# Performance work log

Hardware: AMD Instinct MI355X
Metric: run time of the kernel (lower is better)

The kernel has to match this reference:

```python
import jax, jax.numpy as jnp
import numpy as np

N = 16384      # number of points
DIM = 128      # feature dim
POS_DIM = 3
K = 16         # neighbors (init kwarg k)
SCALE = np.float32(np.sqrt(DIM))


def setup_inputs() -> dict:
    key = jax.random.key(0)
    ks = jax.random.split(key, 16)
    g = lambda i, shape: (jax.random.normal(ks[i], shape, dtype=jnp.float32) * 0.05)
    return {
        "x": jax.random.normal(ks[0], (N, DIM), dtype=jnp.float32),
        "pos": jax.random.uniform(ks[1], (N, POS_DIM), dtype=jnp.float32),
        # weights stored as (in, out); torch Linear applies x @ W.T + b
        "Wq": g(2, (DIM, DIM)),
        "Wk": g(3, (DIM, DIM)),
        "Wv": g(4, (DIM, DIM)),
        "mid_w1": g(5, (DIM, DIM)), "mid_b1": g(6, (DIM,)),
        "mid_w2": g(7, (DIM, DIM)), "mid_b2": g(8, (DIM,)),
        "pe_w1": g(9, (POS_DIM, DIM)), "pe_b1": g(10, (DIM,)),
        "pe_w2": g(11, (DIM, DIM)), "pe_b2": g(12, (DIM,)),
        "fin_w": g(13, (DIM, DIM)), "fin_b": g(14, (DIM,)),
    }


def _knn_indices(pos):
    # squared pairwise distances [N, N]; top-K smallest -> neighbor indices [N, K]
    sq = jnp.sum(pos * pos, axis=-1)
    d2 = sq[:, None] + sq[None, :] - 2.0 * (pos @ pos.T)
    _, ind = jax.lax.top_k(-d2, K)
    return ind


def reference(x, pos, Wq, Wk, Wv, mid_w1, mid_b1, mid_w2, mid_b2,
              pe_w1, pe_b1, pe_w2, pe_b2, fin_w, fin_b):
    ind = _knn_indices(pos)                    # [N, K] int32 (constant wrt grads)
    x_k = x[ind]                               # [N, K, D]
    pos_k = pos[ind]                           # [N, K, 3]
    rel = pos[:, None, :] - pos_k              # [N, K, 3]
    pe = jax.nn.relu(rel @ pe_w1 + pe_b1) @ pe_w2 + pe_b2    # [N, K, D]
    q = x @ Wq                                 # [N, D]
    h = q[:, None, :] - (x_k @ Wk) + pe        # [N, K, D]
    y = jax.nn.relu(h @ mid_w1 + mid_b1) @ mid_w2 + mid_b2   # [N, K, D]
    y = jax.nn.softmax(y / SCALE, axis=-2)     # softmax over neighbors K
    z = x_k @ Wv + pe                          # [N, K, D]
    agg = jnp.sum(y * z, axis=-2)              # [N, D]
    return agg @ fin_w + fin_b + x
```

## Files before the change

kernel.cpp:

```cpp
#include <hip/hip_runtime.h>
#include <hip/hip_bf16.h>

#define N_PTS 16384
#define DIMF  128
#define KNB   16
#define GRES  8
#define NCELL (GRES*GRES*GRES)

typedef __attribute__((ext_vector_type(8))) short bf16x8;
typedef __attribute__((ext_vector_type(4))) short bf16x4;
typedef __attribute__((ext_vector_type(4))) float f32x4;
typedef __attribute__((ext_vector_type(4))) unsigned int u32x4;
typedef __attribute__((ext_vector_type(2))) unsigned int u32x2;

__device__ __forceinline__ unsigned short f2b(float f){
  unsigned int u = __float_as_uint(f);
  u = u + 0x7fffu + ((u >> 16) & 1u);
  return (unsigned short)(u >> 16);
}
__device__ __forceinline__ unsigned cvtpk(float lo, float hi){
  unsigned r;
  asm("v_cvt_pk_bf16_f32 %0, %1, %2" : "=v"(r) : "v"(lo), "v"(hi));
  return r;
}
__device__ __forceinline__ float b2f(unsigned short u){
  return __uint_as_float(((unsigned)u) << 16);
}
__device__ __forceinline__ float b2fs(short s){
  return __uint_as_float(((unsigned)(unsigned short)s) << 16);
}
__device__ __forceinline__ float unsort_f(unsigned s){
  unsigned u = (s & 0x80000000u) ? (s ^ 0x80000000u) : ~s;
  return __uint_as_float(u);
}

__global__ __launch_bounds__(256) void count_kernel(const float* __restrict__ pos, int* __restrict__ cnt){
  int i = blockIdx.x*256 + threadIdx.x;
  float px = pos[i*3+0], py = pos[i*3+1], pz = pos[i*3+2];
  int cx = min(GRES-1, max(0,(int)(px*(float)GRES)));
  int cy = min(GRES-1, max(0,(int)(py*(float)GRES)));
  int cz = min(GRES-1, max(0,(int)(pz*(float)GRES)));
  atomicAdd(&cnt[(cz*GRES+cy)*GRES+cx], 1);
}

__global__ __launch_bounds__(256) void scan_kernel(const int* __restrict__ cnt, int* __restrict__ starts, int* __restrict__ fillp){
  __shared__ int wsum[4];
  int t = threadIdx.x;
  int lane = t & 63, w = t >> 6;
  int a = cnt[2*t], b = cnt[2*t+1];
  int s = a + b;
  int p = s;
  #pragma unroll
  for (int off = 1; off < 64; off <<= 1){
    int v = __shfl_up(p, off, 64);
    if (lane >= off) p += v;
  }
  if (lane == 63) wsum[w] = p;
  __syncthreads();
  int base = 0;
  for (int i = 0; i < w; ++i) base += wsum[i];
  int excl = base + p - s;
  starts[2*t]   = excl;     fillp[2*t]   = excl;
  starts[2*t+1] = excl + a; fillp[2*t+1] = excl + a;
}

__global__ __launch_bounds__(256) void scatter_pack(const float* __restrict__ pos, int* __restrict__ fillp,
                                                    float4* __restrict__ pos4, int* __restrict__ pidx,
                                                    int* __restrict__ inv,
                                                    const float* __restrict__ w0, const float* __restrict__ w1,
                                                    const float* __restrict__ w2, const float* __restrict__ w3,
                                                    const float* __restrict__ w4, const float* __restrict__ w5,
                                                    const float* __restrict__ w6,
                                                    short* __restrict__ dst){
  if (blockIdx.x < 64){
    int i = blockIdx.x*256 + threadIdx.x;
    float px = pos[i*3+0], py = pos[i*3+1], pz = pos[i*3+2];
    int cx = min(GRES-1, max(0,(int)(px*(float)GRES)));
    int cy = min(GRES-1, max(0,(int)(py*(float)GRES)));
    int cz = min(GRES-1, max(0,(int)(pz*(float)GRES)));
    int c = (cz*GRES+cy)*GRES+cx;
    float sq = __fadd_rn(__fadd_rn(__fmul_rn(px,px), __fmul_rn(py,py)), __fmul_rn(pz,pz));
    int s = atomicAdd(&fillp[c], 1);
    pos4[s] = make_float4(px, py, pz, sq);
    pidx[s] = i;
    inv[i] = s;
  } else {
    int pb = blockIdx.x - 64;
    int slot = pb >> 6;
    const float* src = (slot==0)?w0:(slot==1)?w1:(slot==2)?w2:(slot==3)?w3:(slot==4)?w4:(slot==5)?w5:w6;
    int f = (pb & 63)*256 + threadIdx.x;
    int j  = f & 7;
    int ln = (f >> 3) & 63;
    int ks = (f >> 9) & 3;
    int nt = f >> 11;
    int k = ks*32 + ((ln >> 4) << 3) + j;
    int n = nt*16 + (ln & 15);
    dst[slot*16384 + f] = (short)f2b(src[k*DIMF + n]);
  }
}

__global__ __launch_bounds__(256) void knn_query64(const float4* __restrict__ pos4, const int* __restrict__ pidx,
                                                   const int* __restrict__ starts, const int* __restrict__ cnt,
                                                   const int* __restrict__ inv,
                                                   int* __restrict__ ind_slot){
  __shared__ unsigned long long cand[4][64];
  int lane = threadIdx.x & 63;
  int wv   = threadIdx.x >> 6;
  int t = blockIdx.x*4 + wv;
  float4 qp = pos4[t];
  float qx = qp.x, qy = qp.y, qz = qp.z, qsq = qp.w;
  int cx = min(GRES-1, max(0,(int)(qx*(float)GRES)));
  int cy = min(GRES-1, max(0,(int)(qy*(float)GRES)));
  int cz = min(GRES-1, max(0,(int)(qz*(float)GRES)));
  int zlo = max(0,cz-1), zhi = min(GRES-1,cz+1);
  int ylo = max(0,cy-1), yhi = min(GRES-1,cy+1);
  int xlo = max(0,cx-1), xhi = min(GRES-1,cx+1);
  const double h = 0.125;
  double dqx=(double)qx, dqy=(double)qy, dqz=(double)qz;

  int nb = 0;
  if (lane < 27){
    int dz = lane/9 - 1, dy = (lane/3)%3 - 1, dx = lane%3 - 1;
    int zz = cz+dz, yy = cy+dy, xx = cx+dx;
    if (zz>=zlo && zz<=zhi && yy>=ylo && yy<=yhi && xx>=xlo && xx<=xhi)
      nb = cnt[(zz*GRES+yy)*GRES+xx];
  }
  #pragma unroll
  for (int o=1;o<64;o<<=1) nb += __shfl_xor(nb, o, 64);
  float V = (float)((zhi-zlo+1)*(yhi-ylo+1)*(xhi-xlo+1)) * 0.001953125f;
  float r3 = 3.8197186f * V / (float)nb;
  float tau2 = 2.0f * __powf(r3, 0.66666667f);

  int nfound = 0;
  bool okscan = false;
  for (int it = 0; it < 8; ++it){
    nfound = 0;
    for (int zz=zlo; zz<=zhi; ++zz)
    for (int yy=ylo; yy<=yhi; ++yy)
    for (int xx=xlo; xx<=xhi; ++xx){
      double mdx = fmax(0.0, fmax((double)xx*h - dqx, dqx - (double)(xx+1)*h));
      double mdy = fmax(0.0, fmax((double)yy*h - dqy, dqy - (double)(yy+1)*h));
      double mdz = fmax(0.0, fmax((double)zz*h - dqz, dqz - (double)(zz+1)*h));
      double md2 = mdx*mdx + mdy*mdy + mdz*mdz;
      if (md2 > (double)tau2 + 1.0e-5) continue;
      int c = (zz*GRES+yy)*GRES+xx;
      int s0 = starts[c], n = cnt[c];
      for (int b = 0; b < n; b += 64){
        int o = b + lane;
        bool valid = o < n;
        float d = 3.0e38f; int idx = 0;
        if (valid){
          float4 pc = pos4[s0+o];
          idx = pidx[s0+o];
          float dot = __fmaf_rn(qz, pc.z, __fmaf_rn(qy, pc.y, __fmul_rn(qx, pc.x)));
          d   = __fsub_rn(__fadd_rn(qsq, pc.w), __fmul_rn(2.0f, dot));
        }
        bool admit = valid && (d < tau2);
        unsigned long long mask = __ballot(admit);
        if (admit){
          int pos = nfound + (int)__popcll(mask & ((1ull<<lane)-1ull));
          if (pos < 64){
            unsigned su = __float_as_uint(d);
            su ^= (unsigned)((int)su >> 31) | 0x80000000u;
            cand[wv][pos] = ((unsigned long long)su << 32) | (unsigned)idx;
          }
        }
        nfound += (int)__popcll(mask);
      }
    }
    if (nfound > 64){ tau2 *= 0.7f; continue; }
    if (nfound < 16){ tau2 *= 2.0f; continue; }
    okscan = true; break;
  }

  bool needfb = !okscan;
  if (okscan){
    asm volatile("s_waitcnt lgkmcnt(0)" ::: "memory");
    __builtin_amdgcn_sched_barrier(0);
    unsigned long long key = (lane < nfound) ? cand[wv][lane] : ~0ull;

    #pragma unroll
    for (int k = 2; k <= 64; k <<= 1){
      #pragma unroll
      for (int j = k>>1; j >= 1; j >>= 1){
        unsigned long long other = __shfl_xor(key, j, 64);
        bool takeSmall = (((lane & k) == 0) != ((lane & j) != 0));
        bool less = other < key;
        key = (takeSmall == less) ? other : key;
      }
    }
    if (lane < 16) ind_slot[t*KNB + lane] = inv[(int)(unsigned)(key & 0xffffffffu)];

    unsigned long long k15 = __shfl(key, 15, 64);
    float b16 = unsort_f((unsigned)(k15 >> 32));
    double mg = 1.0e300;
    if (cx-1 > 0)      mg = fmin(mg, dqx - (double)(cx-1)*h);
    if (cx+1 < GRES-1) mg = fmin(mg, (double)(cx+2)*h - dqx);
    if (cy-1 > 0)      mg = fmin(mg, dqy - (double)(cy-1)*h);
    if (cy+1 < GRES-1) mg = fmin(mg, (double)(cy+2)*h - dqy);
    if (cz-1 > 0)      mg = fmin(mg, dqz - (double)(cz-1)*h);
    if (cz+1 < GRES-1) mg = fmin(mg, (double)(cz+2)*h - dqz);
    needfb = !(mg*mg > (double)b16 + 1.0e-5);
  }

  if (needfb){
    float bd[KNB]; int bi[KNB];
    #pragma unroll
    for (int k=0;k<KNB;++k){ bd[k] = 3.0e38f; bi[k] = 0x7fffffff; }
    for (int r = 0; r < GRES; ++r){
      int zl = max(0, cz-r), zh = min(GRES-1, cz+r);
      int yl = max(0, cy-r), yh = min(GRES-1, cy+r);
      int xl = max(0, cx-r), xh = min(GRES-1, cx+r);
      for (int zz = zl; zz <= zh; ++zz)
      for (int yy = yl; yy <= yh; ++yy)
      for (int xx = xl; xx <= xh; ++xx){
        int ring = max(abs(zz-cz), max(abs(yy-cy), abs(xx-cx)));
        if (ring != r) continue;
        int c = (zz*GRES+yy)*GRES+xx;
        int s0 = starts[c], e = s0 + cnt[c];
        for (int s = s0; s < e; ++s){
          float4 pc = pos4[s];
          int idx = pidx[s];
          float dot = __fmaf_rn(qz, pc.z, __fmaf_rn(qy, pc.y, __fmul_rn(qx, pc.x)));
          float d   = __fsub_rn(__fadd_rn(qsq, pc.w), __fmul_rn(2.0f, dot));
          bool adm = (d < bd[KNB-1]) || (d == bd[KNB-1] && idx < bi[KNB-1]);
          if (adm){
            #pragma unroll
            for (int p = KNB-1; p >= 1; --p){
              float pd = bd[p-1]; int pi = bi[p-1];
              bool sh  = (pd > d) || (pd == d && pi > idx);
              bool ins = (!sh) && ((bd[p] > d) || (bd[p] == d && bi[p] > idx));
              bd[p] = sh ? pd : (ins ? d   : bd[p]);
              bi[p] = sh ? pi : (ins ? idx : bi[p]);
            }
            bool s0b = (bd[0] > d) || (bd[0] == d && bi[0] > idx);
            if (s0b){ bd[0] = d; bi[0] = idx; }
          }
        }
      }
      if (bd[KNB-1] < 3.0e37f){
        double mg = 1.0e300;
        if (cx - r > 0)      mg = fmin(mg, dqx - (double)(cx-r)*h);
        if (cx + r < GRES-1) mg = fmin(mg, (double)(cx+r+1)*h - dqx);
        if (cy - r > 0)      mg = fmin(mg, dqy - (double)(cy-r)*h);
        if (cy + r < GRES-1) mg = fmin(mg, (double)(cy+r+1)*h - dqy);
        if (cz - r > 0)      mg = fmin(mg, dqz - (double)(cz-r)*h);
        if (cz + r < GRES-1) mg = fmin(mg, (double)(cz+r+1)*h - dqz);
        if (mg*mg > (double)bd[KNB-1] + 1.0e-5) break;
      }
    }
    if (lane < 16) ind_slot[t*KNB + lane] = inv[bi[lane]];
  }
}

__global__ __launch_bounds__(256) void proj_kernel(const float* __restrict__ x, const int* __restrict__ pidx,
                                                   const short* __restrict__ pw,
                                                   unsigned short* __restrict__ q, unsigned short* __restrict__ xk,
                                                   unsigned short* __restrict__ xv){
  __shared__ __align__(16) char Abuf[8192];
  int tid = threadIdx.x, lane = tid & 63, wv = tid >> 6;
  int r0 = blockIdx.x * 32;
  {
    int row = tid >> 3, seg = tid & 7;
    int orig = pidx[r0 + row];
    const float4* xr = (const float4*)(x + (size_t)orig*DIMF + seg*16);
    float4 a = xr[0], b = xr[1], c = xr[2], d = xr[3];
    u32x4 u0, u1;
    u0[0] = cvtpk(a.x, a.y); u0[1] = cvtpk(a.z, a.w);
    u0[2] = cvtpk(b.x, b.y); u0[3] = cvtpk(b.z, b.w);
    u1[0] = cvtpk(c.x, c.y); u1[1] = cvtpk(c.z, c.w);
    u1[2] = cvtpk(d.x, d.y); u1[3] = cvtpk(d.z, d.w);
    *(u32x4*)(&Abuf[row*256 + ((seg*32 +  0) ^ ((row&7)<<4))]) = u0;
    *(u32x4*)(&Abuf[row*256 + ((seg*32 + 16) ^ ((row&7)<<4))]) = u1;
  }
  __syncthreads();
  int mt = wv >> 1;
  int nh = (wv & 1) * 4;
  #pragma unroll 1
  for (int w = 0; w < 3; ++w){
    const bf16x8* bw = (const bf16x8*)(pw + w*16384);
    unsigned short* dst = (w==0) ? q : (w==1) ? xk : xv;
    f32x4 acc[4];
    #pragma unroll
    for (int n=0;n<4;++n) acc[n] = (f32x4){0.f,0.f,0.f,0.f};
    #pragma unroll
    for (int ks=0;ks<4;++ks){
      int ra = mt*16 + (lane&15);
      int cb = ks*64 + ((lane>>4)<<4);
      bf16x8 a0 = *(const bf16x8*)(&Abuf[ra*256 + (cb ^ ((ra&7)<<4))]);
      #pragma unroll
      for (int n=0;n<4;++n){
        bf16x8 b = bw[((nh+n)*4+ks)*64 + lane];
        acc[n] = __builtin_amdgcn_mfma_f32_16x16x32_bf16(a0, b, acc[n], 0, 0, 0);
      }
    }
    #pragma unroll
    for (int n=0;n<4;++n){
      int grow = r0 + mt*16 + ((lane>>4)<<2);
      int col = (nh+n)*16 + (lane&15);
      unsigned pk01 = cvtpk(acc[n][0], acc[n][1]);
      unsigned pk23 = cvtpk(acc[n][2], acc[n][3]);
      dst[(size_t)(grow+0)*DIMF + col] = (unsigned short)pk01;
      dst[(size_t)(grow+1)*DIMF + col] = (unsigned short)(pk01 >> 16);
      dst[(size_t)(grow+2)*DIMF + col] = (unsigned short)pk23;
      dst[(size_t)(grow+3)*DIMF + col] = (unsigned short)(pk23 >> 16);
    }
  }
}

__global__ __launch_bounds__(512, 2) void main_kernel(
    const float* __restrict__ x, const float4* __restrict__ pos4, const int* __restrict__ pidx,
    const float* __restrict__ pe_w1, const float* __restrict__ pe_b1, const float* __restrict__ pe_b2,
    const float* __restrict__ mid_b1, const float* __restrict__ mid_b2, const float* __restrict__ fin_b,
    const unsigned short* __restrict__ qarr, const unsigned short* __restrict__ xkarr,
    const unsigned short* __restrict__ xvarr,
    const int* __restrict__ ind_slot, const short* __restrict__ pw,
    float* __restrict__ out)
{
  __shared__ __align__(16) char peLDS[32768];
  __shared__ __align__(16) char wbuf[32768];
  __shared__ float aggT[DIMF][9];
  __shared__ int indbuf[128];
  __shared__ int origbuf[8];
  int tid = threadIdx.x;
  int lane = tid & 63;
  int wv = tid >> 6;
  int swz = (blockIdx.x & 7) * (N_PTS/8/8) + (blockIdx.x >> 3);
  int t0 = swz * 8;

  int g = lane >> 4, kl = lane & 15;
  int mt = wv;

  #define STAGE_W(slot) { \
    const char* gsrc = (const char*)(pw + (size_t)(slot)*16384) + wv*4096 + lane*16; \
    char* ldst = &wbuf[wv*4096]; \
    __builtin_amdgcn_global_load_lds(gsrc,        ldst,        16, 0, 0); \
    __builtin_amdgcn_global_load_lds(gsrc + 1024, ldst + 1024, 16, 0, 0); \
    __builtin_amdgcn_global_load_lds(gsrc + 2048, ldst + 2048, 16, 0, 0); \
    __builtin_amdgcn_global_load_lds(gsrc + 3072, ldst + 3072, 16, 0, 0); }

  if (tid < 128) indbuf[tid] = ind_slot[swz*128 + tid];
  if (tid < 8) origbuf[tid] = pidx[t0 + tid];
  STAGE_W(3);
  __syncthreads();

  int nb4[4];
  #pragma unroll
  for (int r=0;r<4;++r) nb4[r] = indbuf[mt*16 + g*4 + r];
  int nbr = indbuf[mt*16 + kl];
  unsigned short zraw[8][4];
  #pragma unroll
  for (int nt=0;nt<8;++nt)
    #pragma unroll
    for (int r=0;r<4;++r)
      zraw[nt][r] = xvarr[(size_t)nb4[r]*DIMF + nt*16 + kl];

  bf16x8 tfrag[4];
  {
    float4 pq = pos4[t0+mt];
    float4 pn = pos4[nbr];
    float rx = pq.x-pn.x, ry = pq.y-pn.y, rz = pq.z-pn.z;
    #pragma unroll
    for (int ks=0;ks<4;++ks){
      int c0 = ks*32 + g*8;
      const float4* w0 = (const float4*)(pe_w1 + c0);
      const float4* w1 = (const float4*)(pe_w1 + DIMF + c0);
      const float4* w2 = (const float4*)(pe_w1 + 2*DIMF + c0);
      const float4* bb = (const float4*)(pe_b1 + c0);
      float4 wa0=w0[0], wa1=w0[1], wb0=w1[0], wb1=w1[1], wc0=w2[0], wc1=w2[1], wd0=bb[0], wd1=bb[1];
      float wa[8]={wa0.x,wa0.y,wa0.z,wa0.w,wa1.x,wa1.y,wa1.z,wa1.w};
      float wb[8]={wb0.x,wb0.y,wb0.z,wb0.w,wb1.x,wb1.y,wb1.z,wb1.w};
      float wc[8]={wc0.x,wc0.y,wc0.z,wc0.w,wc1.x,wc1.y,wc1.z,wc1.w};
      float wd[8]={wd0.x,wd0.y,wd0.z,wd0.w,wd1.x,wd1.y,wd1.z,wd1.w};
      float tv[8];
      #pragma unroll
      for (int j=0;j<8;++j)
        tv[j] = fmaxf(fmaf(rx, wa[j], fmaf(ry, wb[j], fmaf(rz, wc[j], wd[j]))), 0.f);
      u32x4 u;
      u[0] = cvtpk(tv[0], tv[1]); u[1] = cvtpk(tv[2], tv[3]);
      u[2] = cvtpk(tv[4], tv[5]); u[3] = cvtpk(tv[6], tv[7]);
      tfrag[ks] = __builtin_bit_cast(bf16x8, u);
    }
  }

  f32x4 acc[8];
  const bf16x8* bw = (const bf16x8*)wbuf;

  {
    #pragma unroll
    for (int nt=0;nt<8;++nt){
      float bv = pe_b2[nt*16 + kl];
      acc[nt] = (f32x4){bv,bv,bv,bv};
    }
    #pragma unroll
    for (int ks=0;ks<4;++ks){
      #pragma unroll
      for (int nt=0;nt<8;++nt){
        bf16x8 b = bw[(nt*4+ks)*64 + lane];
        acc[nt] = __builtin_amdgcn_mfma_f32_16x16x32_bf16(tfrag[ks], b, acc[nt], 0, 0, 0);
      }
    }
  }

  bf16x4 zb[8];
  int r0w = mt*16 + g*4;
  #pragma unroll
  for (int nt=0;nt<8;++nt){
    int col = nt*16 + kl;
    float p0 = acc[nt][0], p1 = acc[nt][1], p2 = acc[nt][2], p3 = acc[nt][3];
    unsigned pk01 = cvtpk(p0, p1), pk23 = cvtpk(p2, p3);
    *(unsigned short*)&peLDS[(r0w+0)*256 + ((col*2) ^ (((r0w+0)&7)<<4))] = (unsigned short)pk01;
    *(unsigned short*)&peLDS[(r0w+1)*256 + ((col*2) ^ (((r0w+1)&7)<<4))] = (unsigned short)(pk01 >> 16);
    *(unsigned short*)&peLDS[(r0w+2)*256 + ((col*2) ^ (((r0w+2)&7)<<4))] = (unsigned short)pk23;
    *(unsigned short*)&peLDS[(r0w+3)*256 + ((col*2) ^ (((r0w+3)&7)<<4))] = (unsigned short)(pk23 >> 16);
    float z0 = b2f(zraw[nt][0]) + p0;
    float z1 = b2f(zraw[nt][1]) + p1;
    float z2 = b2f(zraw[nt][2]) + p2;
    float z3 = b2f(zraw[nt][3]) + p3;
    u32x2 zu; zu[0] = cvtpk(z0, z1); zu[1] = cvtpk(z2, z3);
    zb[nt] = __builtin_bit_cast(bf16x4, zu);
  }

  bf16x8 q8[4], k8[4];
  {
    const unsigned short* qrow = qarr + (size_t)(t0+mt)*DIMF;
    const unsigned short* krow = xkarr + (size_t)nbr*DIMF;
    #pragma unroll
    for (int ks=0;ks<4;++ks){
      int c0 = ks*32 + g*8;
      q8[ks] = *(const bf16x8*)(qrow + c0);
      k8[ks] = *(const bf16x8*)(krow + c0);
    }
  }
  __syncthreads();
  STAGE_W(4);

  bf16x8 hfrag[4];
  {
    int row = mt*16 + kl;
    #pragma unroll
    for (int ks=0;ks<4;++ks){
      int c0 = ks*32 + g*8;
      bf16x8 p8 = *(const bf16x8*)(&peLDS[row*256 + ((c0*2) ^ ((row&7)<<4))]);
      float hf[8];
      #pragma unroll
      for (int j=0;j<8;++j)
        hf[j] = (b2fs(q8[ks][j]) - b2fs(k8[ks][j])) + b2fs(p8[j]);
      u32x4 u;
      u[0] = cvtpk(hf[0], hf[1]); u[1] = cvtpk(hf[2], hf[3]);
      u[2] = cvtpk(hf[4], hf[5]); u[3] = cvtpk(hf[6], hf[7]);
      hfrag[ks] = __builtin_bit_cast(bf16x8, u);
    }
  }
  __syncthreads();

  {
    #pragma unroll
    for (int nt=0;nt<8;++nt){
      float bv = mid_b1[nt*16 + kl];
      acc[nt] = (f32x4){bv,bv,bv,bv};
    }
    #pragma unroll
    for (int ks=0;ks<4;++ks){
      #pragma unroll
      for (int nt=0;nt<8;++nt){
        bf16x8 b = bw[(nt*4+ks)*64 + lane];
        acc[nt] = __builtin_amdgcn_mfma_f32_16x16x32_bf16(hfrag[ks], b, acc[nt], 0, 0, 0);
      }
    }
  }
  __syncthreads();
  STAGE_W(5);
  #pragma unroll
  for (int nt=0;nt<8;++nt){
    int col = nt*16 + kl;
    unsigned pk01 = cvtpk(fmaxf(acc[nt][0],0.f), fmaxf(acc[nt][1],0.f));
    unsigned pk23 = cvtpk(fmaxf(acc[nt][2],0.f), fmaxf(acc[nt][3],0.f));
    *(unsigned short*)&peLDS[(r0w+0)*256 + ((col*2) ^ (((r0w+0)&7)<<4))] = (unsigned short)pk01;
    *(unsigned short*)&peLDS[(r0w+1)*256 + ((col*2) ^ (((r0w+1)&7)<<4))] = (unsigned short)(pk01 >> 16);
    *(unsigned short*)&peLDS[(r0w+2)*256 + ((col*2) ^ (((r0w+2)&7)<<4))] = (unsigned short)pk23;
    *(unsigned short*)&peLDS[(r0w+3)*256 + ((col*2) ^ (((r0w+3)&7)<<4))] = (unsigned short)(pk23 >> 16);
  }
  __syncthreads();

  {
    #pragma unroll
    for (int nt=0;nt<8;++nt){
      float bv = mid_b2[nt*16 + kl];
      acc[nt] = (f32x4){bv,bv,bv,bv};
    }
    #pragma unroll
    for (int ks=0;ks<4;++ks){
      int ra = mt*16 + kl;
      int cb = ks*64 + g*16;
      bf16x8 a0 = *(const bf16x8*)(&peLDS[ra*256 + (cb ^ ((ra&7)<<4))]);
      #pragma unroll
      for (int nt=0;nt<8;++nt){
        bf16x8 b = bw[(nt*4+ks)*64 + lane];
        acc[nt] = __builtin_amdgcn_mfma_f32_16x16x32_bf16(a0, b, acc[nt], 0, 0, 0);
      }
    }
  }
  __syncthreads();
  STAGE_W(6);

  {
    const float invS = 0.08838834764831843f;
    #pragma unroll
    for (int nt=0;nt<8;++nt){
      f32x4 y = acc[nt];
      float mx = fmaxf(fmaxf(y[0],y[1]), fmaxf(y[2],y[3]));
      mx = fmaxf(mx, __shfl_xor(mx, 16, 64));
      mx = fmaxf(mx, __shfl_xor(mx, 32, 64));
      float e0 = __expf((y[0]-mx)*invS);
      float e1 = __expf((y[1]-mx)*invS);
      float e2 = __expf((y[2]-mx)*invS);
      float e3 = __expf((y[3]-mx)*invS);
      float ssum = e0+e1+e2+e3;
      ssum += __shfl_xor(ssum, 16, 64);
      ssum += __shfl_xor(ssum, 32, 64);
      bf16x4 zv = zb[nt];
      float ps = (e0*b2fs(zv[0]) + e1*b2fs(zv[1]) + e2*b2fs(zv[2]) + e3*b2fs(zv[3])) / ssum;
      ps += __shfl_xor(ps, 16, 64);
      ps += __shfl_xor(ps, 32, 64);
      if (lane < 16) aggT[nt*16 + lane][mt] = ps;
    }
  }
  __syncthreads();

  {
    f32x4 facc = (f32x4){0.f,0.f,0.f,0.f};
    #pragma unroll
    for (int ks=0;ks<4;++ks){
      int c0 = ks*32 + g*8;
      float av[8];
      #pragma unroll
      for (int j=0;j<8;++j)
        av[j] = (kl < 8) ? aggT[c0+j][kl] : 0.f;
      u32x4 u;
      u[0] = cvtpk(av[0], av[1]); u[1] = cvtpk(av[2], av[3]);
      u[2] = cvtpk(av[4], av[5]); u[3] = cvtpk(av[6], av[7]);
      bf16x8 a = __builtin_bit_cast(bf16x8, u);
      bf16x8 b = bw[(wv*4+ks)*64 + lane];
      facc = __builtin_amdgcn_mfma_f32_16x16x32_bf16(a, b, facc, 0, 0, 0);
    }
    int col = wv*16 + kl;
    float fb = fin_b[col];
    if (g < 2){
      #pragma unroll
      for (int r=0;r<4;++r){
        int prow = g*4 + r;
        int o = origbuf[prow];
        out[(size_t)o*DIMF + col] = facc[r] + fb + x[(size_t)o*DIMF + col];
      }
    }
  }
  #undef STAGE_W
}

extern "C" void kernel_launch(void* const* d_in, const int* in_sizes, int n_in,
                              void* d_out, int out_size, void* d_ws, size_t ws_size,
                              hipStream_t stream)
{
  (void)in_sizes; (void)n_in; (void)out_size; (void)ws_size;
  const float* x      = (const float*)d_in[0];
  const float* pos    = (const float*)d_in[1];
  const float* Wq     = (const float*)d_in[2];
  const float* Wk     = (const float*)d_in[3];
  const float* Wv     = (const float*)d_in[4];
  const float* mid_w1 = (const float*)d_in[5];
  const float* mid_b1 = (const float*)d_in[6];
  const float* mid_w2 = (const float*)d_in[7];
  const float* mid_b2 = (const float*)d_in[8];
  const float* pe_w1  = (const float*)d_in[9];
  const float* pe_b1  = (const float*)d_in[10];
  const float* pe_w2  = (const float*)d_in[11];
  const float* pe_b2  = (const float*)d_in[12];
  const float* fin_w  = (const float*)d_in[13];
  const float* fin_b  = (const float*)d_in[14];
  float* out = (float*)d_out;
  char* ws = (char*)d_ws;

  int*    cellcnt = (int*)   (ws + 0);
  int*    fillp   = (int*)   (ws + 4096);
  int*    starts  = (int*)   (ws + 8192);
  int*    pidx    = (int*)   (ws + 49152);
  float4* pos4    = (float4*)(ws + 114688);
  int*    ind     = (int*)   (ws + 376832);
  short*  pw      = (short*) (ws + 1425408);
  int*    inv     = (int*)   (ws + 1654784);
  unsigned short* qarr  = (unsigned short*)(ws + 1720320);
  unsigned short* xkarr = (unsigned short*)(ws + 5914624);
  unsigned short* xvarr = (unsigned short*)(ws + 10108928);

  hipMemsetAsync(cellcnt, 0, NCELL*sizeof(int), stream);
  count_kernel  <<<N_PTS/256, 256, 0, stream>>>(pos, cellcnt);
  scan_kernel   <<<1,         256, 0, stream>>>(cellcnt, starts, fillp);
  scatter_pack  <<<64 + 7*64, 256, 0, stream>>>(pos, fillp, pos4, pidx, inv,
                                                Wq, Wk, Wv, pe_w2, mid_w1, mid_w2, fin_w, pw);
  knn_query64   <<<N_PTS/4,   256, 0, stream>>>(pos4, pidx, starts, cellcnt, inv, ind);
  proj_kernel   <<<N_PTS/32,  256, 0, stream>>>(x, pidx, pw, qarr, xkarr, xvarr);
  main_kernel   <<<N_PTS/8,   512, 0, stream>>>(x, pos4, pidx, pe_w1, pe_b1, pe_b2, mid_b1, mid_b2, fin_b,
                                                qarr, xkarr, xvarr, ind, pw, out);
}
```

Before: 157.2 us.

## Fuse grid-based kNN search into main kernel, removing separate kNN launch

The grid-cell kNN query is moved from its own kernel into the start of main_kernel. Each of the 8 waves finds the neighbours for one query point and writes the indices straight into the LDS index buffer, instead of writing them to global memory for a later reload. This removes one kernel launch and the global round trip of the neighbour index array. In exchange, main_kernel takes on the kNN register and control-flow load and 4KB more LDS, which may lower occupancy and lengthen the main kernel's prologue.

```diff
diff --git a/kernel.cpp b/kernel.cpp
--- a/kernel.cpp
+++ b/kernel.cpp
@@ -99,160 +99,6 @@
   }
 }
 
-__global__ __launch_bounds__(256) void knn_query64(const float4* __restrict__ pos4, const int* __restrict__ pidx,
-                                                   const int* __restrict__ starts, const int* __restrict__ cnt,
-                                                   const int* __restrict__ inv,
-                                                   int* __restrict__ ind_slot){
-  __shared__ unsigned long long cand[4][64];
-  int lane = threadIdx.x & 63;
-  int wv   = threadIdx.x >> 6;
-  int t = blockIdx.x*4 + wv;
-  float4 qp = pos4[t];
-  float qx = qp.x, qy = qp.y, qz = qp.z, qsq = qp.w;
-  int cx = min(GRES-1, max(0,(int)(qx*(float)GRES)));
-  int cy = min(GRES-1, max(0,(int)(qy*(float)GRES)));
-  int cz = min(GRES-1, max(0,(int)(qz*(float)GRES)));
-  int zlo = max(0,cz-1), zhi = min(GRES-1,cz+1);
-  int ylo = max(0,cy-1), yhi = min(GRES-1,cy+1);
-  int xlo = max(0,cx-1), xhi = min(GRES-1,cx+1);
-  const double h = 0.125;
-  double dqx=(double)qx, dqy=(double)qy, dqz=(double)qz;
-
-  int nb = 0;
-  if (lane < 27){
-    int dz = lane/9 - 1, dy = (lane/3)%3 - 1, dx = lane%3 - 1;
-    int zz = cz+dz, yy = cy+dy, xx = cx+dx;
-    if (zz>=zlo && zz<=zhi && yy>=ylo && yy<=yhi && xx>=xlo && xx<=xhi)
-      nb = cnt[(zz*GRES+yy)*GRES+xx];
-  }
-  #pragma unroll
-  for (int o=1;o<64;o<<=1) nb += __shfl_xor(nb, o, 64);
-  float V = (float)((zhi-zlo+1)*(yhi-ylo+1)*(xhi-xlo+1)) * 0.001953125f;
-  float r3 = 3.8197186f * V / (float)nb;
-  float tau2 = 2.0f * __powf(r3, 0.66666667f);
-
-  int nfound = 0;
-  bool okscan = false;
-  for (int it = 0; it < 8; ++it){
-    nfound = 0;
-    for (int zz=zlo; zz<=zhi; ++zz)
-    for (int yy=ylo; yy<=yhi; ++yy)
-    for (int xx=xlo; xx<=xhi; ++xx){
-      double mdx = fmax(0.0, fmax((double)xx*h - dqx, dqx - (double)(xx+1)*h));
-      double mdy = fmax(0.0, fmax((double)yy*h - dqy, dqy - (double)(yy+1)*h));
-      double mdz = fmax(0.0, fmax((double)zz*h - dqz, dqz - (double)(zz+1)*h));
-      double md2 = mdx*mdx + mdy*mdy + mdz*mdz;
-      if (md2 > (double)tau2 + 1.0e-5) continue;
-      int c = (zz*GRES+yy)*GRES+xx;
-      int s0 = starts[c], n = cnt[c];
-      for (int b = 0; b < n; b += 64){
-        int o = b + lane;
-        bool valid = o < n;
-        float d = 3.0e38f; int idx = 0;
-        if (valid){
-          float4 pc = pos4[s0+o];
-          idx = pidx[s0+o];
-          float dot = __fmaf_rn(qz, pc.z, __fmaf_rn(qy, pc.y, __fmul_rn(qx, pc.x)));
-          d   = __fsub_rn(__fadd_rn(qsq, pc.w), __fmul_rn(2.0f, dot));
-        }
-        bool admit = valid && (d < tau2);
-        unsigned long long mask = __ballot(admit);
-        if (admit){
-          int pos = nfound + (int)__popcll(mask & ((1ull<<lane)-1ull));
-          if (pos < 64){
-            unsigned su = __float_as_uint(d);
-            su ^= (unsigned)((int)su >> 31) | 0x80000000u;
-            cand[wv][pos] = ((unsigned long long)su << 32) | (unsigned)idx;
-          }
-        }
-        nfound += (int)__popcll(mask);
-      }
-    }
-    if (nfound > 64){ tau2 *= 0.7f; continue; }
-    if (nfound < 16){ tau2 *= 2.0f; continue; }
-    okscan = true; break;
-  }
-
-  bool needfb = !okscan;
-  if (okscan){
-    asm volatile("s_waitcnt lgkmcnt(0)" ::: "memory");
-    __builtin_amdgcn_sched_barrier(0);
-    unsigned long long key = (lane < nfound) ? cand[wv][lane] : ~0ull;
-
-    #pragma unroll
-    for (int k = 2; k <= 64; k <<= 1){
-      #pragma unroll
-      for (int j = k>>1; j >= 1; j >>= 1){
-        unsigned long long other = __shfl_xor(key, j, 64);
-        bool takeSmall = (((lane & k) == 0) != ((lane & j) != 0));
-        bool less = other < key;
-        key = (takeSmall == less) ? other : key;
-      }
-    }
-    if (lane < 16) ind_slot[t*KNB + lane] = inv[(int)(unsigned)(key & 0xffffffffu)];
-
-    unsigned long long k15 = __shfl(key, 15, 64);
-    float b16 = unsort_f((unsigned)(k15 >> 32));
-    double mg = 1.0e300;
-    if (cx-1 > 0)      mg = fmin(mg, dqx - (double)(cx-1)*h);
-    if (cx+1 < GRES-1) mg = fmin(mg, (double)(cx+2)*h - dqx);
-    if (cy-1 > 0)      mg = fmin(mg, dqy - (double)(cy-1)*h);
-    if (cy+1 < GRES-1) mg = fmin(mg, (double)(cy+2)*h - dqy);
-    if (cz-1 > 0)      mg = fmin(mg, dqz - (double)(cz-1)*h);
-    if (cz+1 < GRES-1) mg = fmin(mg, (double)(cz+2)*h - dqz);
-    needfb = !(mg*mg > (double)b16 + 1.0e-5);
-  }
-
-  if (needfb){
-    float bd[KNB]; int bi[KNB];
-    #pragma unroll
-    for (int k=0;k<KNB;++k){ bd[k] = 3.0e38f; bi[k] = 0x7fffffff; }
-    for (int r = 0; r < GRES; ++r){
-      int zl = max(0, cz-r), zh = min(GRES-1, cz+r);
-      int yl = max(0, cy-r), yh = min(GRES-1, cy+r);
-      int xl = max(0, cx-r), xh = min(GRES-1, cx+r);
-      for (int zz = zl; zz <= zh; ++zz)
-      for (int yy = yl; yy <= yh; ++yy)
-      for (int xx = xl; xx <= xh; ++xx){
-        int ring = max(abs(zz-cz), max(abs(yy-cy), abs(xx-cx)));
-        if (ring != r) continue;
-        int c = (zz*GRES+yy)*GRES+xx;
-        int s0 = starts[c], e = s0 + cnt[c];
-        for (int s = s0; s < e; ++s){
-          float4 pc = pos4[s];
-          int idx = pidx[s];
-          float dot = __fmaf_rn(qz, pc.z, __fmaf_rn(qy, pc.y, __fmul_rn(qx, pc.x)));
-          float d   = __fsub_rn(__fadd_rn(qsq, pc.w), __fmul_rn(2.0f, dot));
-          bool adm = (d < bd[KNB-1]) || (d == bd[KNB-1] && idx < bi[KNB-1]);
-          if (adm){
-            #pragma unroll
-            for (int p = KNB-1; p >= 1; --p){
-              float pd = bd[p-1]; int pi = bi[p-1];
-              bool sh  = (pd > d) || (pd == d && pi > idx);
-              bool ins = (!sh) && ((bd[p] > d) || (bd[p] == d && bi[p] > idx));
-              bd[p] = sh ? pd : (ins ? d   : bd[p]);
-              bi[p] = sh ? pi : (ins ? idx : bi[p]);
-            }
-            bool s0b = (bd[0] > d) || (bd[0] == d && bi[0] > idx);
-            if (s0b){ bd[0] = d; bi[0] = idx; }
-          }
-        }
-      }
-      if (bd[KNB-1] < 3.0e37f){
-        double mg = 1.0e300;
-        if (cx - r > 0)      mg = fmin(mg, dqx - (double)(cx-r)*h);
-        if (cx + r < GRES-1) mg = fmin(mg, (double)(cx+r+1)*h - dqx);
-        if (cy - r > 0)      mg = fmin(mg, dqy - (double)(cy-r)*h);
-        if (cy + r < GRES-1) mg = fmin(mg, (double)(cy+r+1)*h - dqy);
-        if (cz - r > 0)      mg = fmin(mg, dqz - (double)(cz-r)*h);
-        if (cz + r < GRES-1) mg = fmin(mg, (double)(cz+r+1)*h - dqz);
-        if (mg*mg > (double)bd[KNB-1] + 1.0e-5) break;
-      }
-    }
-    if (lane < 16) ind_slot[t*KNB + lane] = inv[bi[lane]];
-  }
-}
-
 __global__ __launch_bounds__(256) void proj_kernel(const float* __restrict__ x, const int* __restrict__ pidx,
                                                    const short* __restrict__ pw,
                                                    unsigned short* __restrict__ q, unsigned short* __restrict__ xk,
@@ -310,15 +156,17 @@
 
 __global__ __launch_bounds__(512, 2) void main_kernel(
     const float* __restrict__ x, const float4* __restrict__ pos4, const int* __restrict__ pidx,
+    const int* __restrict__ starts, const int* __restrict__ cnt, const int* __restrict__ inv,
     const float* __restrict__ pe_w1, const float* __restrict__ pe_b1, const float* __restrict__ pe_b2,
     const float* __restrict__ mid_b1, const float* __restrict__ mid_b2, const float* __restrict__ fin_b,
     const unsigned short* __restrict__ qarr, const unsigned short* __restrict__ xkarr,
     const unsigned short* __restrict__ xvarr,
-    const int* __restrict__ ind_slot, const short* __restrict__ pw,
+    const short* __restrict__ pw,
     float* __restrict__ out)
 {
   __shared__ __align__(16) char peLDS[32768];
   __shared__ __align__(16) char wbuf[32768];
+  __shared__ unsigned long long cand2[8][64];
   __shared__ float aggT[DIMF][9];
   __shared__ int indbuf[128];
   __shared__ int origbuf[8];
@@ -331,6 +179,156 @@
   int g = lane >> 4, kl = lane & 15;
   int mt = wv;
 
+  {
+    int t = t0 + wv;
+    float4 qp = pos4[t];
+    float qx = qp.x, qy = qp.y, qz = qp.z, qsq = qp.w;
+    int cx = min(GRES-1, max(0,(int)(qx*(float)GRES)));
+    int cy = min(GRES-1, max(0,(int)(qy*(float)GRES)));
+    int cz = min(GRES-1, max(0,(int)(qz*(float)GRES)));
+    int zlo = max(0,cz-1), zhi = min(GRES-1,cz+1);
+    int ylo = max(0,cy-1), yhi = min(GRES-1,cy+1);
+    int xlo = max(0,cx-1), xhi = min(GRES-1,cx+1);
+    const double h = 0.125;
+    double dqx=(double)qx, dqy=(double)qy, dqz=(double)qz;
+
+    int nb = 0;
+    if (lane < 27){
+      int dz = lane/9 - 1, dy = (lane/3)%3 - 1, dx = lane%3 - 1;
+      int zz = cz+dz, yy = cy+dy, xx = cx+dx;
+      if (zz>=zlo && zz<=zhi && yy>=ylo && yy<=yhi && xx>=xlo && xx<=xhi)
+        nb = cnt[(zz*GRES+yy)*GRES+xx];
+    }
+    #pragma unroll
+    for (int o=1;o<64;o<<=1) nb += __shfl_xor(nb, o, 64);
+    float V = (float)((zhi-zlo+1)*(yhi-ylo+1)*(xhi-xlo+1)) * 0.001953125f;
+    float r3 = 3.8197186f * V / (float)nb;
+    float tau2 = 2.0f * __powf(r3, 0.66666667f);
+
+    int nfound = 0;
+    bool okscan = false;
+    for (int it = 0; it < 8; ++it){
+      nfound = 0;
+      for (int zz=zlo; zz<=zhi; ++zz)
+      for (int yy=ylo; yy<=yhi; ++yy)
+      for (int xx=xlo; xx<=xhi; ++xx){
+        double mdx = fmax(0.0, fmax((double)xx*h - dqx, dqx - (double)(xx+1)*h));
+        double mdy = fmax(0.0, fmax((double)yy*h - dqy, dqy - (double)(yy+1)*h));
+        double mdz = fmax(0.0, fmax((double)zz*h - dqz, dqz - (double)(zz+1)*h));
+        double md2 = mdx*mdx + mdy*mdy + mdz*mdz;
+        if (md2 > (double)tau2 + 1.0e-5) continue;
+        int c = (zz*GRES+yy)*GRES+xx;
+        int s0 = starts[c], n = cnt[c];
+        for (int b = 0; b < n; b += 64){
+          int o = b + lane;
+          bool valid = o < n;
+          float d = 3.0e38f; int idx = 0;
+          if (valid){
+            float4 pc = pos4[s0+o];
+            idx = pidx[s0+o];
+            float dot = __fmaf_rn(qz, pc.z, __fmaf_rn(qy, pc.y, __fmul_rn(qx, pc.x)));
+            d   = __fsub_rn(__fadd_rn(qsq, pc.w), __fmul_rn(2.0f, dot));
+          }
+          bool admit = valid && (d < tau2);
+          unsigned long long mask = __ballot(admit);
+          if (admit){
+            int pos = nfound + (int)__popcll(mask & ((1ull<<lane)-1ull));
+            if (pos < 64){
+              unsigned su = __float_as_uint(d);
+              su ^= (unsigned)((int)su >> 31) | 0x80000000u;
+              cand2[wv][pos] = ((unsigned long long)su << 32) | (unsigned)idx;
+            }
+          }
+          nfound += (int)__popcll(mask);
+        }
+      }
+      if (nfound > 64){ tau2 *= 0.7f; continue; }
+      if (nfound < 16){ tau2 *= 2.0f; continue; }
+      okscan = true; break;
+    }
+
+    bool needfb = !okscan;
+    if (okscan){
+      asm volatile("s_waitcnt lgkmcnt(0)" ::: "memory");
+      __builtin_amdgcn_sched_barrier(0);
+      unsigned long long key = (lane < nfound) ? cand2[wv][lane] : ~0ull;
+
+      #pragma unroll
+      for (int k = 2; k <= 64; k <<= 1){
+        #pragma unroll
+        for (int j = k>>1; j >= 1; j >>= 1){
+          unsigned long long other = __shfl_xor(key, j, 64);
+          bool takeSmall = (((lane & k) == 0) != ((lane & j) != 0));
+          bool less = other < key;
+          key = (takeSmall == less) ? other : key;
+        }
+      }
+      if (lane < 16) indbuf[wv*KNB + lane] = inv[(int)(unsigned)(key & 0xffffffffu)];
+
+      unsigned long long k15 = __shfl(key, 15, 64);
+      float b16 = unsort_f((unsigned)(k15 >> 32));
+      double mg = 1.0e300;
+      if (cx-1 > 0)      mg = fmin(mg, dqx - (double)(cx-1)*h);
+      if (cx+1 < GRES-1) mg = fmin(mg, (double)(cx+2)*h - dqx);
+      if (cy-1 > 0)      mg = fmin(mg, dqy - (double)(cy-1)*h);
+      if (cy+1 < GRES-1) mg = fmin(mg, (double)(cy+2)*h - dqy);
+      if (cz-1 > 0)      mg = fmin(mg, dqz - (double)(cz-1)*h);
+      if (cz+1 < GRES-1) mg = fmin(mg, (double)(cz+2)*h - dqz);
+      needfb = !(mg*mg > (double)b16 + 1.0e-5);
+    }
+
+    if (needfb){
+      float bd[KNB]; int bi[KNB];
+      #pragma unroll
+      for (int k=0;k<KNB;++k){ bd[k] = 3.0e38f; bi[k] = 0x7fffffff; }
+      for (int r = 0; r < GRES; ++r){
+        int zl = max(0, cz-r), zh = min(GRES-1, cz+r);
+        int yl = max(0, cy-r), yh = min(GRES-1, cy+r);
+        int xl = max(0, cx-r), xh = min(GRES-1, cx+r);
+        for (int zz = zl; zz <= zh; ++zz)
+        for (int yy = yl; yy <= yh; ++yy)
+        for (int xx = xl; xx <= xh; ++xx){
+          int ring = max(abs(zz-cz), max(abs(yy-cy), abs(xx-cx)));
+          if (ring != r) continue;
+          int c = (zz*GRES+yy)*GRES+xx;
+          int s0 = starts[c], e = s0 + cnt[c];
+          for (int s = s0; s < e; ++s){
+            float4 pc = pos4[s];
+            int idx = pidx[s];
+            float dot = __fmaf_rn(qz, pc.z, __fmaf_rn(qy, pc.y, __fmul_rn(qx, pc.x)));
+            float d   = __fsub_rn(__fadd_rn(qsq, pc.w), __fmul_rn(2.0f, dot));
+            bool adm = (d < bd[KNB-1]) || (d == bd[KNB-1] && idx < bi[KNB-1]);
+            if (adm){
+              #pragma unroll
+              for (int p = KNB-1; p >= 1; --p){
+                float pd = bd[p-1]; int pi = bi[p-1];
+                bool sh  = (pd > d) || (pd == d && pi > idx);
+                bool ins = (!sh) && ((bd[p] > d) || (bd[p] == d && bi[p] > idx));
+                bd[p] = sh ? pd : (ins ? d   : bd[p]);
+                bi[p] = sh ? pi : (ins ? idx : bi[p]);
+              }
+              bool s0b = (bd[0] > d) || (bd[0] == d && bi[0] > idx);
+              if (s0b){ bd[0] = d; bi[0] = idx; }
+            }
+          }
+        }
+        if (bd[KNB-1] < 3.0e37f){
+          double mg = 1.0e300;
+          if (cx - r > 0)      mg = fmin(mg, dqx - (double)(cx-r)*h);
+          if (cx + r < GRES-1) mg = fmin(mg, (double)(cx+r+1)*h - dqx);
+          if (cy - r > 0)      mg = fmin(mg, dqy - (double)(cy-r)*h);
+          if (cy + r < GRES-1) mg = fmin(mg, (double)(cy+r+1)*h - dqy);
+          if (cz - r > 0)      mg = fmin(mg, dqz - (double)(cz-r)*h);
+          if (cz + r < GRES-1) mg = fmin(mg, (double)(cz+r+1)*h - dqz);
+          if (mg*mg > (double)bd[KNB-1] + 1.0e-5) break;
+        }
+      }
+      if (lane < 16) indbuf[wv*KNB + lane] = inv[bi[lane]];
+    }
+  }
+
+  if (tid < 8) origbuf[tid] = pidx[t0 + tid];
+  STAGE_W_DECL:;
   #define STAGE_W(slot) { \
     const char* gsrc = (const char*)(pw + (size_t)(slot)*16384) + wv*4096 + lane*16; \
     char* ldst = &wbuf[wv*4096]; \
@@ -339,8 +337,6 @@
     __builtin_amdgcn_global_load_lds(gsrc + 2048, ldst + 2048, 16, 0, 0); \
     __builtin_amdgcn_global_load_lds(gsrc + 3072, ldst + 3072, 16, 0, 0); }
 
-  if (tid < 128) indbuf[tid] = ind_slot[swz*128 + tid];
-  if (tid < 8) origbuf[tid] = pidx[t0 + tid];
   STAGE_W(3);
   __syncthreads();
 
@@ -586,7 +582,6 @@
   int*    starts  = (int*)   (ws + 8192);
   int*    pidx    = (int*)   (ws + 49152);
   float4* pos4    = (float4*)(ws + 114688);
-  int*    ind     = (int*)   (ws + 376832);
   short*  pw      = (short*) (ws + 1425408);
   int*    inv     = (int*)   (ws + 1654784);
   unsigned short* qarr  = (unsigned short*)(ws + 1720320);
@@ -598,8 +593,8 @@
   scan_kernel   <<<1,         256, 0, stream>>>(cellcnt, starts, fillp);
   scatter_pack  <<<64 + 7*64, 256, 0, stream>>>(pos, fillp, pos4, pidx, inv,
                                                 Wq, Wk, Wv, pe_w2, mid_w1, mid_w2, fin_w, pw);
-  knn_query64   <<<N_PTS/4,   256, 0, stream>>>(pos4, pidx, starts, cellcnt, inv, ind);
   proj_kernel   <<<N_PTS/32,  256, 0, stream>>>(x, pidx, pw, qarr, xkarr, xvarr);
-  main_kernel   <<<N_PTS/8,   512, 0, stream>>>(x, pos4, pidx, pe_w1, pe_b1, pe_b2, mid_b1, mid_b2, fin_b,
-                                                qarr, xkarr, xvarr, ind, pw, out);
-}
+  main_kernel   <<<N_PTS/8,   512, 0, stream>>>(x, pos4, pidx, starts, cellcnt, inv,
+                                                pe_w1, pe_b1, pe_b2, mid_b1, mid_b2, fin_b,
+                                                qarr, xkarr, xvarr, pw, out);
+}
```

Result: no change. 157.3 us (+0.1%).
